# Kernel optimization log

Hardware: AMD Instinct MI355X
Metric: run time of the kernel (lower is better)

## Reference

```python
import jax, jax.numpy as jnp
import numpy as np

EMBED = 64
HEADS = 4
HEAD_DIM = EMBED // HEADS
N, T = 1024, 36


def setup_inputs() -> dict:
    key = jax.random.key(0)
    ks = jax.random.split(key, 8)
    scale = 1.0 / np.sqrt(HEAD_DIM)
    return {
        "values": jax.random.normal(ks[0], (N, T, EMBED), dtype=jnp.float32),
        "keys": jax.random.normal(ks[1], (N, T, EMBED), dtype=jnp.float32),
        "query": jax.random.normal(ks[2], (N, T, EMBED), dtype=jnp.float32),
        "Wv": jax.random.normal(ks[3], (HEAD_DIM, HEAD_DIM), dtype=jnp.float32) * scale,
        "Wk": jax.random.normal(ks[4], (HEAD_DIM, HEAD_DIM), dtype=jnp.float32) * scale,
        "Wq": jax.random.normal(ks[5], (HEAD_DIM, HEAD_DIM), dtype=jnp.float32) * scale,
        "Wo": jax.random.normal(ks[6], (EMBED, EMBED), dtype=jnp.float32) * (1.0 / np.sqrt(EMBED)),
        "bo": jax.random.normal(ks[7], (EMBED,), dtype=jnp.float32) * 0.01,
    }


def reference(values, keys, query, Wv, Wk, Wq, Wo, bo):
    n, t, c = query.shape
    h, d = HEADS, HEAD_DIM
    v = values.reshape(n, t, h, d)
    k = keys.reshape(n, t, h, d)
    q = query.reshape(n, t, h, d)
    # nn.Linear(head_dim, head_dim, bias=False): x @ W.T
    v = jnp.einsum('nthd,ed->nthe', v, Wv)
    k = jnp.einsum('nthd,ed->nthe', k, Wk)
    q = jnp.einsum('nthd,ed->nthe', q, Wq)
    # attention over the node dim: energy [N_q, N_k, T, H]
    energy = jnp.einsum('qthd,kthd->qkth', q, k)
    attention = jax.nn.softmax(energy / jnp.sqrt(jnp.float32(c)), axis=1)
    out = jnp.einsum('qkth,kthd->qthd', attention, v).reshape(n, t, h * d)
    return out @ Wo.T + bo
```

## Files before the change

### kernel.cpp

```cpp
#include <hip/hip_runtime.h>
#include <math.h>

#define N_NODES 1024
#define T_STEPS 36
#define KTILE   128
#define KSTR2   24
#define VTSTR   136
#define WOS     72
#define OBS2    72
#define YSTR    67

typedef __bf16  bf16x8 __attribute__((ext_vector_type(8)));
typedef float   f32x4  __attribute__((ext_vector_type(4)));

#define MFMA_BF16 __builtin_amdgcn_mfma_f32_16x16x32_bf16
#define PERM_HI 0x07060302u
#define PERM_LO 0x05040100u

__device__ __forceinline__ unsigned short bf16_rne(float f) {
    unsigned int u = __float_as_uint(f);
    u += 0x7FFFu + ((u >> 16) & 1u);
    return (unsigned short)(u >> 16);
}
__device__ __forceinline__ float bf16_tof(unsigned short h) {
    return __uint_as_float(((unsigned int)h) << 16);
}
__device__ __forceinline__ unsigned int bf16_bias(float f) {
    unsigned int u = __float_as_uint(f);
    return u + 0x7FFFu + ((u >> 16) & 1u);
}
__device__ __forceinline__ unsigned int split_pack(float a) {
    unsigned short hi = bf16_rne(a);
    unsigned short lo = bf16_rne(a - bf16_tof(hi));
    return ((unsigned int)hi << 16) | lo;
}

__global__ __launch_bounds__(128) void proj5_kernel(
    const float* __restrict__ vin, const float* __restrict__ kin, const float* __restrict__ qin,
    const float* __restrict__ Wv, const float* __restrict__ Wk, const float* __restrict__ Wq,
    unsigned short* __restrict__ qhi, unsigned short* __restrict__ qlo,
    unsigned short* __restrict__ khi, unsigned short* __restrict__ klo,
    unsigned short* __restrict__ vthi, unsigned short* __restrict__ vtlo)
{
    __shared__ float sW[256];
    __shared__ unsigned int ys[128 * YSTR];

    const int tid = threadIdx.x;
    const int mat = blockIdx.y;
    const int nt  = blockIdx.x & 15;
    const int tt  = blockIdx.x >> 4;
    const int n0  = nt * 64, t0 = tt * 2;

    const float* in = (mat == 0) ? vin : (mat == 1) ? kin : qin;
    const float* W  = (mat == 0) ? Wv  : (mat == 1) ? Wk  : Wq;
    sW[tid] = W[tid]; sW[tid + 128] = W[tid + 128];
    __syncthreads();

    {
        const int nl = tid >> 1, tl = tid & 1;
        const size_t p = ((size_t)(n0 + nl)) * T_STEPS + (t0 + tl);
        const float4* src = (const float4*)(in + p * 64);
        float x[64];
        #pragma unroll
        for (int i = 0; i < 16; ++i) {
            float4 f = src[i];
            x[4*i] = f.x; x[4*i+1] = f.y; x[4*i+2] = f.z; x[4*i+3] = f.w;
        }
        const float scale = (mat == 2) ? 0.18033688011112042f : 1.0f;
        unsigned int* yrow = &ys[tid * YSTR];
        #pragma unroll
        for (int e = 0; e < 16; ++e) {
            float4 w0 = *(const float4*)&sW[e*16+0],  w1 = *(const float4*)&sW[e*16+4];
            float4 w2 = *(const float4*)&sW[e*16+8],  w3 = *(const float4*)&sW[e*16+12];
            #pragma unroll
            for (int hd = 0; hd < 4; ++hd) {
                const float* xr = &x[hd*16];
                float a = xr[0]*w0.x;
                a = fmaf(xr[1],w0.y,a);  a = fmaf(xr[2],w0.z,a);  a = fmaf(xr[3],w0.w,a);
                a = fmaf(xr[4],w1.x,a);  a = fmaf(xr[5],w1.y,a);  a = fmaf(xr[6],w1.z,a);  a = fmaf(xr[7],w1.w,a);
                a = fmaf(xr[8],w2.x,a);  a = fmaf(xr[9],w2.y,a);  a = fmaf(xr[10],w2.z,a); a = fmaf(xr[11],w2.w,a);
                a = fmaf(xr[12],w3.x,a); a = fmaf(xr[13],w3.y,a); a = fmaf(xr[14],w3.z,a); a = fmaf(xr[15],w3.w,a);
                yrow[hd*16 + e] = split_pack(a * scale);
            }
        }
    }
    __syncthreads();

    if (mat != 0) {
        unsigned short* ohi = (mat == 1) ? khi : qhi;
        unsigned short* olo = (mat == 1) ? klo : qlo;
        const int nl2 = tid >> 1, eh = tid & 1;
        #pragma unroll
        for (int pass = 0; pass < 8; ++pass) {
            const int tl2 = pass & 1, hd = pass >> 1;
            const unsigned int* yr = &ys[(nl2*2 + tl2) * YSTR + hd*16 + eh*8];
            unsigned int u0 = yr[0], u1 = yr[1], u2 = yr[2], u3 = yr[3];
            unsigned int u4 = yr[4], u5 = yr[5], u6 = yr[6], u7 = yr[7];
            uint4 hi4, lo4;
            hi4.x = __builtin_amdgcn_perm(u1, u0, PERM_HI);
            hi4.y = __builtin_amdgcn_perm(u3, u2, PERM_HI);
            hi4.z = __builtin_amdgcn_perm(u5, u4, PERM_HI);
            hi4.w = __builtin_amdgcn_perm(u7, u6, PERM_HI);
            lo4.x = __builtin_amdgcn_perm(u1, u0, PERM_LO);
            lo4.y = __builtin_amdgcn_perm(u3, u2, PERM_LO);
            lo4.z = __builtin_amdgcn_perm(u5, u4, PERM_LO);
            lo4.w = __builtin_amdgcn_perm(u7, u6, PERM_LO);
            const int th = (t0 + tl2) * 4 + hd;
            const size_t off = ((size_t)th * N_NODES + n0 + nl2) * 16 + eh * 8;
            *(uint4*)(ohi + off) = hi4;
            *(uint4*)(olo + off) = lo4;
        }
    } else {
        const int e = tid >> 3, ng = tid & 7;
        #pragma unroll
        for (int pass = 0; pass < 8; ++pass) {
            const int tl2 = pass & 1, hd = pass >> 1;
            unsigned int u[8];
            #pragma unroll
            for (int j = 0; j < 8; ++j)
                u[j] = ys[((ng*8 + j)*2 + tl2) * YSTR + hd*16 + e];
            uint4 hi4, lo4;
            hi4.x = __builtin_amdgcn_perm(u[1], u[0], PERM_HI);
            hi4.y = __builtin_amdgcn_perm(u[3], u[2], PERM_HI);
            hi4.z = __builtin_amdgcn_perm(u[5], u[4], PERM_HI);
            hi4.w = __builtin_amdgcn_perm(u[7], u[6], PERM_HI);
            lo4.x = __builtin_amdgcn_perm(u[1], u[0], PERM_LO);
            lo4.y = __builtin_amdgcn_perm(u[3], u[2], PERM_LO);
            lo4.z = __builtin_amdgcn_perm(u[5], u[4], PERM_LO);
            lo4.w = __builtin_amdgcn_perm(u[7], u[6], PERM_LO);
            const int th = (t0 + tl2) * 4 + hd;
            const size_t off = ((size_t)th * 16 + e) * N_NODES + n0 + ng * 8;
            *(uint4*)(vthi + off) = hi4;
            *(uint4*)(vtlo + off) = lo4;
        }
    }
}

__global__ __launch_bounds__(256, 4) void attn_mfma3_kernel(
    const unsigned short* __restrict__ qhi, const unsigned short* __restrict__ qlo,
    const unsigned short* __restrict__ khi, const unsigned short* __restrict__ klo,
    const unsigned short* __restrict__ vthi, const unsigned short* __restrict__ vtlo,
    unsigned short* __restrict__ obh, unsigned short* __restrict__ obl)
{
    __shared__ unsigned short khi_s[KTILE * KSTR2];
    __shared__ unsigned short klo_s[KTILE * KSTR2];
    __shared__ unsigned short vthi_s[16 * VTSTR];
    __shared__ unsigned short vtlo_s[16 * VTSTR];

    const int tid  = threadIdx.x;
    const int wave = tid >> 6, lane = tid & 63;
    const int m = lane & 15, quad = lane >> 4;

    const int bid = blockIdx.x;
    const int th  = bid % 144;
    const int qb  = bid / 144;
    const int t   = th >> 2, hd = th & 3;
    const int q0  = qb * 128;
    const size_t base_th = (size_t)th * N_NODES;

    const bf16x8 bzero = {};
    bf16x8 b1q[2], b2q[2];
    #pragma unroll
    for (int g = 0; g < 2; ++g) {
        const int qrow = q0 + wave * 32 + g * 16 + m;
        b1q[g] = *(const bf16x8*)(qhi + (base_th + qrow) * 16 + (quad & 1) * 8);
        b2q[g] = (quad < 2)
            ? *(const bf16x8*)(qlo + (base_th + qrow) * 16 + (quad & 1) * 8) : bzero;
    }

    f32x4 og[2] = {{0.f,0.f,0.f,0.f},{0.f,0.f,0.f,0.f}};
    float lsum[2] = {0.f, 0.f};
    const unsigned short* kbase = (quad < 2) ? khi_s : klo_s;
    const int koff = m * KSTR2 + (quad & 1) * 8;
    const int voff = m * VTSTR + quad * 8;

    for (int kt = 0; kt < N_NODES; kt += KTILE) {
        __syncthreads();
        if (tid < 128) {
            const int r = tid;
            const uint4* gh = (const uint4*)(khi + (base_th + kt + r) * 16);
            const uint4* gl = (const uint4*)(klo + (base_th + kt + r) * 16);
            uint4 a0 = gh[0], a1 = gh[1], c0 = gl[0], c1 = gl[1];
            *(uint4*)&khi_s[r * KSTR2]     = a0;
            *(uint4*)&khi_s[r * KSTR2 + 8] = a1;
            *(uint4*)&klo_s[r * KSTR2]     = c0;
            *(uint4*)&klo_s[r * KSTR2 + 8] = c1;
        } else {
            const int j = tid - 128;
            const int sel = j >> 6, d = (j >> 2) & 15, part = j & 3;
            const unsigned short* src = (sel ? vtlo : vthi)
                + ((size_t)th * 16 + d) * N_NODES + kt + part * 32;
            unsigned short* dst = (sel ? vtlo_s : vthi_s) + d * VTSTR + part * 32;
            uint4 a0 = ((const uint4*)src)[0], a1 = ((const uint4*)src)[1];
            uint4 a2 = ((const uint4*)src)[2], a3 = ((const uint4*)src)[3];
            *(uint2*)&dst[0]  = make_uint2(a0.x, a0.y);
            *(uint2*)&dst[8]  = make_uint2(a0.z, a0.w);
            *(uint2*)&dst[16] = make_uint2(a1.x, a1.y);
            *(uint2*)&dst[24] = make_uint2(a1.z, a1.w);
            *(uint2*)&dst[4]  = make_uint2(a2.x, a2.y);
            *(uint2*)&dst[12] = make_uint2(a2.z, a2.w);
            *(uint2*)&dst[20] = make_uint2(a3.x, a3.y);
            *(uint2*)&dst[28] = make_uint2(a3.z, a3.w);
        }
        __syncthreads();

        #pragma unroll
        for (int c = 0; c < 4; ++c) {
            bf16x8 a0 = *(const bf16x8*)(kbase + (2*c    ) * 16 * KSTR2 + koff);
            bf16x8 a1 = *(const bf16x8*)(kbase + (2*c + 1) * 16 * KSTR2 + koff);
            unsigned int pk[2][4];
            #pragma unroll
            for (int g = 0; g < 2; ++g) {
                f32x4 s0 = MFMA_BF16(a0, b1q[g], (f32x4){0.f,0.f,0.f,0.f}, 0, 0, 0);
                s0 = MFMA_BF16(a0, b2q[g], s0, 0, 0, 0);
                f32x4 s1 = MFMA_BF16(a1, b1q[g], (f32x4){0.f,0.f,0.f,0.f}, 0, 0, 0);
                s1 = MFMA_BF16(a1, b2q[g], s1, 0, 0, 0);
                unsigned int u[8];
                float ls = 0.f;
                #pragma unroll
                for (int r = 0; r < 4; ++r) {
                    u[r]   = bf16_bias(__builtin_amdgcn_exp2f(s0[r]));
                    u[4+r] = bf16_bias(__builtin_amdgcn_exp2f(s1[r]));
                    ls += __uint_as_float(u[r]   & 0xFFFF0000u);
                    ls += __uint_as_float(u[4+r] & 0xFFFF0000u);
                }
                lsum[g] += ls;
                pk[g][0] = __builtin_amdgcn_perm(u[1], u[0], PERM_HI);
                pk[g][1] = __builtin_amdgcn_perm(u[3], u[2], PERM_HI);
                pk[g][2] = __builtin_amdgcn_perm(u[5], u[4], PERM_HI);
                pk[g][3] = __builtin_amdgcn_perm(u[7], u[6], PERM_HI);
            }
            bf16x8 vh = *(const bf16x8*)&vthi_s[voff + c * 32];
            bf16x8 vl = *(const bf16x8*)&vtlo_s[voff + c * 32];
            #pragma unroll
            for (int g = 0; g < 2; ++g) {
                union { unsigned int u[4]; bf16x8 v; } ap;
                ap.u[0] = pk[g][0]; ap.u[1] = pk[g][1];
                ap.u[2] = pk[g][2]; ap.u[3] = pk[g][3];
                og[g] = MFMA_BF16(ap.v, vh, og[g], 0, 0, 0);
                og[g] = MFMA_BF16(ap.v, vl, og[g], 0, 0, 0);
            }
        }
    }

    #pragma unroll
    for (int g = 0; g < 2; ++g) {
        lsum[g] += __shfl_xor(lsum[g], 16);
        lsum[g] += __shfl_xor(lsum[g], 32);
        #pragma unroll
        for (int r = 0; r < 4; ++r) {
            const float l = __shfl(lsum[g], quad * 4 + r);
            const float val = og[g][r] / l;
            const int row = q0 + wave * 32 + g * 16 + quad * 4 + r;
            const size_t off = ((size_t)row * T_STEPS + t) * 64 + hd * 16 + m;
            unsigned short hh = bf16_rne(val);
            obh[off] = hh;
            obl[off] = bf16_rne(val - bf16_tof(hh));
        }
    }
}

__global__ __launch_bounds__(256) void outproj_mfma_kernel(
    const unsigned short* __restrict__ obh, const unsigned short* __restrict__ obl,
    const float* __restrict__ Wo, const float* __restrict__ bo,
    float* __restrict__ out)
{
    __shared__ unsigned short woh[64 * WOS], wol[64 * WOS];
    __shared__ unsigned short oth[64 * OBS2], otl[64 * OBS2];
    __shared__ float sb[64];
    const int tid = threadIdx.x;

    #pragma unroll
    for (int i = 0; i < 16; ++i) {
        int idx = tid + 256 * i;
        int r = idx >> 6, c = idx & 63;
        float w = Wo[idx];
        unsigned short hh = bf16_rne(w);
        woh[r * WOS + c] = hh;
        wol[r * WOS + c] = bf16_rne(w - bf16_tof(hh));
    }
    if (tid < 64) sb[tid] = bo[tid];

    const size_t p0 = (size_t)blockIdx.x * 64;
    #pragma unroll
    for (int i = 0; i < 2; ++i) {
        int idx = tid + 256 * i;
        int r = idx >> 3, c = (idx & 7) * 8;
        *(uint4*)&oth[r * OBS2 + c] = *(const uint4*)(obh + (p0 + r) * 64 + c);
        *(uint4*)&otl[r * OBS2 + c] = *(const uint4*)(obl + (p0 + r) * 64 + c);
    }
    __syncthreads();

    const int wave = tid >> 6, lane = tid & 63;
    const int m = lane & 15, quad = lane >> 4;
    const int r0 = wave * 16;

    bf16x8 ah[2], al[2];
    #pragma unroll
    for (int kh = 0; kh < 2; ++kh) {
        ah[kh] = *(const bf16x8*)&oth[(r0 + m) * OBS2 + kh * 32 + quad * 8];
        al[kh] = *(const bf16x8*)&otl[(r0 + m) * OBS2 + kh * 32 + quad * 8];
    }

    f32x4 acc[4] = {{0,0,0,0},{0,0,0,0},{0,0,0,0},{0,0,0,0}};
    #pragma unroll
    for (int jt = 0; jt < 4; ++jt) {
        #pragma unroll
        for (int kh = 0; kh < 2; ++kh) {
            bf16x8 bh = *(const bf16x8*)&woh[(jt * 16 + m) * WOS + kh * 32 + quad * 8];
            bf16x8 bl = *(const bf16x8*)&wol[(jt * 16 + m) * WOS + kh * 32 + quad * 8];
            acc[jt] = MFMA_BF16(ah[kh], bh, acc[jt], 0, 0, 0);
            acc[jt] = MFMA_BF16(al[kh], bh, acc[jt], 0, 0, 0);
            acc[jt] = MFMA_BF16(ah[kh], bl, acc[jt], 0, 0, 0);
        }
    }

    #pragma unroll
    for (int jt = 0; jt < 4; ++jt) {
        const float b = sb[jt * 16 + m];
        #pragma unroll
        for (int r = 0; r < 4; ++r)
            out[(p0 + r0 + quad * 4 + r) * 64 + jt * 16 + m] = acc[jt][r] + b;
    }
}

extern "C" void kernel_launch(void* const* d_in, const int* in_sizes, int n_in,
                              void* d_out, int out_size, void* d_ws, size_t ws_size,
                              hipStream_t stream)
{
    (void)in_sizes; (void)n_in; (void)out_size; (void)ws_size;
    const float* values = (const float*)d_in[0];
    const float* keys   = (const float*)d_in[1];
    const float* query  = (const float*)d_in[2];
    const float* Wv     = (const float*)d_in[3];
    const float* Wk     = (const float*)d_in[4];
    const float* Wq     = (const float*)d_in[5];
    const float* Wo     = (const float*)d_in[6];
    const float* bo     = (const float*)d_in[7];

    const size_t TOT = (size_t)144 * N_NODES * 16;
    unsigned short* ws16 = (unsigned short*)d_ws;
    unsigned short* qhi  = ws16;
    unsigned short* qlo  = ws16 + 1*TOT;
    unsigned short* khi  = ws16 + 2*TOT;
    unsigned short* klo  = ws16 + 3*TOT;
    unsigned short* vthi = ws16 + 4*TOT;
    unsigned short* vtlo = ws16 + 5*TOT;
    unsigned short* obh  = ws16 + 6*TOT;
    unsigned short* obl  = ws16 + 7*TOT;

    proj5_kernel<<<dim3(288, 3), 128, 0, stream>>>(values, keys, query, Wv, Wk, Wq,
                                                   qhi, qlo, khi, klo, vthi, vtlo);
    attn_mfma3_kernel<<<dim3(8 * 144), 256, 0, stream>>>(qhi, qlo, khi, klo, vthi, vtlo,
                                                         obh, obl);
    outproj_mfma_kernel<<<dim3(576), 256, 0, stream>>>(obh, obl, Wo, bo, (float*)d_out);
}
```

Baseline: 145.9 us.

## Compute softmax row sums with MFMA against ones and halve attention block size

Row sums of the exponentials are now accumulated by an extra MFMA against a vector of bf16 ones, replacing the scalar adds and the cross-lane shuffles. The bias-add rounding and perm packing are replaced by direct __bf16 conversions. Blocks shrink to 128 threads and 64 queries each, with twice as many blocks, and both threads load K and V tiles. The trade-off is fewer queries sharing each K/V tile, which doubles K/V shared-memory staging traffic, plus one extra MFMA per group. The final division becomes a fast reciprocal multiply.

```diff
diff --git a/kernel.cpp b/kernel.cpp
--- a/kernel.cpp
+++ b/kernel.cpp
@@ -24,10 +24,6 @@
 }
 __device__ __forceinline__ float bf16_tof(unsigned short h) {
     return __uint_as_float(((unsigned int)h) << 16);
-}
-__device__ __forceinline__ unsigned int bf16_bias(float f) {
-    unsigned int u = __float_as_uint(f);
-    return u + 0x7FFFu + ((u >> 16) & 1u);
 }
 __device__ __forceinline__ unsigned int split_pack(float a) {
     unsigned short hi = bf16_rne(a);
@@ -136,7 +132,7 @@
     }
 }
 
-__global__ __launch_bounds__(256, 4) void attn_mfma3_kernel(
+__global__ __launch_bounds__(128, 4) void attn_mfma4_kernel(
     const unsigned short* __restrict__ qhi, const unsigned short* __restrict__ qlo,
     const unsigned short* __restrict__ khi, const unsigned short* __restrict__ klo,
     const unsigned short* __restrict__ vthi, const unsigned short* __restrict__ vtlo,
@@ -155,7 +151,7 @@
     const int th  = bid % 144;
     const int qb  = bid / 144;
     const int t   = th >> 2, hd = th & 3;
-    const int q0  = qb * 128;
+    const int q0  = qb * 64;
     const size_t base_th = (size_t)th * N_NODES;
 
     const bf16x8 bzero = {};
@@ -168,39 +164,45 @@
             ? *(const bf16x8*)(qlo + (base_th + qrow) * 16 + (quad & 1) * 8) : bzero;
     }
 
-    f32x4 og[2] = {{0.f,0.f,0.f,0.f},{0.f,0.f,0.f,0.f}};
-    float lsum[2] = {0.f, 0.f};
+    union { unsigned short su[8]; bf16x8 v; } onesu;
+    #pragma unroll
+    for (int i = 0; i < 8; ++i) onesu.su[i] = 0x3F80;
+    const bf16x8 bones = onesu.v;
+
+    f32x4 og[2]   = {{0.f,0.f,0.f,0.f},{0.f,0.f,0.f,0.f}};
+    f32x4 lacc[2] = {{0.f,0.f,0.f,0.f},{0.f,0.f,0.f,0.f}};
     const unsigned short* kbase = (quad < 2) ? khi_s : klo_s;
     const int koff = m * KSTR2 + (quad & 1) * 8;
     const int voff = m * VTSTR + quad * 8;
 
+    const int vsel = tid >> 6, vd = (tid >> 2) & 15, vpart = tid & 3;
+    const unsigned short* vsrc0 = (vsel ? vtlo : vthi)
+        + ((size_t)th * 16 + vd) * N_NODES + vpart * 32;
+    unsigned short* vdst = (vsel ? vtlo_s : vthi_s) + vd * VTSTR + vpart * 32;
+
     for (int kt = 0; kt < N_NODES; kt += KTILE) {
         __syncthreads();
-        if (tid < 128) {
-            const int r = tid;
-            const uint4* gh = (const uint4*)(khi + (base_th + kt + r) * 16);
-            const uint4* gl = (const uint4*)(klo + (base_th + kt + r) * 16);
+        {
+            const uint4* gh = (const uint4*)(khi + (base_th + kt + tid) * 16);
+            const uint4* gl = (const uint4*)(klo + (base_th + kt + tid) * 16);
             uint4 a0 = gh[0], a1 = gh[1], c0 = gl[0], c1 = gl[1];
-            *(uint4*)&khi_s[r * KSTR2]     = a0;
-            *(uint4*)&khi_s[r * KSTR2 + 8] = a1;
-            *(uint4*)&klo_s[r * KSTR2]     = c0;
-            *(uint4*)&klo_s[r * KSTR2 + 8] = c1;
-        } else {
-            const int j = tid - 128;
-            const int sel = j >> 6, d = (j >> 2) & 15, part = j & 3;
-            const unsigned short* src = (sel ? vtlo : vthi)
-                + ((size_t)th * 16 + d) * N_NODES + kt + part * 32;
-            unsigned short* dst = (sel ? vtlo_s : vthi_s) + d * VTSTR + part * 32;
+            *(uint4*)&khi_s[tid * KSTR2]     = a0;
+            *(uint4*)&khi_s[tid * KSTR2 + 8] = a1;
+            *(uint4*)&klo_s[tid * KSTR2]     = c0;
+            *(uint4*)&klo_s[tid * KSTR2 + 8] = c1;
+        }
+        {
+            const unsigned short* src = vsrc0 + kt;
             uint4 a0 = ((const uint4*)src)[0], a1 = ((const uint4*)src)[1];
             uint4 a2 = ((const uint4*)src)[2], a3 = ((const uint4*)src)[3];
-            *(uint2*)&dst[0]  = make_uint2(a0.x, a0.y);
-            *(uint2*)&dst[8]  = make_uint2(a0.z, a0.w);
-            *(uint2*)&dst[16] = make_uint2(a1.x, a1.y);
-            *(uint2*)&dst[24] = make_uint2(a1.z, a1.w);
-            *(uint2*)&dst[4]  = make_uint2(a2.x, a2.y);
-            *(uint2*)&dst[12] = make_uint2(a2.z, a2.w);
-            *(uint2*)&dst[20] = make_uint2(a3.x, a3.y);
-            *(uint2*)&dst[28] = make_uint2(a3.z, a3.w);
+            *(uint2*)&vdst[0]  = make_uint2(a0.x, a0.y);
+            *(uint2*)&vdst[8]  = make_uint2(a0.z, a0.w);
+            *(uint2*)&vdst[16] = make_uint2(a1.x, a1.y);
+            *(uint2*)&vdst[24] = make_uint2(a1.z, a1.w);
+            *(uint2*)&vdst[4]  = make_uint2(a2.x, a2.y);
+            *(uint2*)&vdst[12] = make_uint2(a2.z, a2.w);
+            *(uint2*)&vdst[20] = make_uint2(a3.x, a3.y);
+            *(uint2*)&vdst[28] = make_uint2(a3.z, a3.w);
         }
         __syncthreads();
 
@@ -208,49 +210,35 @@
         for (int c = 0; c < 4; ++c) {
             bf16x8 a0 = *(const bf16x8*)(kbase + (2*c    ) * 16 * KSTR2 + koff);
             bf16x8 a1 = *(const bf16x8*)(kbase + (2*c + 1) * 16 * KSTR2 + koff);
-            unsigned int pk[2][4];
+            bf16x8 vh = *(const bf16x8*)&vthi_s[voff + c * 32];
+            bf16x8 vl = *(const bf16x8*)&vtlo_s[voff + c * 32];
             #pragma unroll
             for (int g = 0; g < 2; ++g) {
                 f32x4 s0 = MFMA_BF16(a0, b1q[g], (f32x4){0.f,0.f,0.f,0.f}, 0, 0, 0);
                 s0 = MFMA_BF16(a0, b2q[g], s0, 0, 0, 0);
                 f32x4 s1 = MFMA_BF16(a1, b1q[g], (f32x4){0.f,0.f,0.f,0.f}, 0, 0, 0);
                 s1 = MFMA_BF16(a1, b2q[g], s1, 0, 0, 0);
-                unsigned int u[8];
-                float ls = 0.f;
-                #pragma unroll
-                for (int r = 0; r < 4; ++r) {
-                    u[r]   = bf16_bias(__builtin_amdgcn_exp2f(s0[r]));
-                    u[4+r] = bf16_bias(__builtin_amdgcn_exp2f(s1[r]));
-                    ls += __uint_as_float(u[r]   & 0xFFFF0000u);
-                    ls += __uint_as_float(u[4+r] & 0xFFFF0000u);
-                }
-                lsum[g] += ls;
-                pk[g][0] = __builtin_amdgcn_perm(u[1], u[0], PERM_HI);
-                pk[g][1] = __builtin_amdgcn_perm(u[3], u[2], PERM_HI);
-                pk[g][2] = __builtin_amdgcn_perm(u[5], u[4], PERM_HI);
-                pk[g][3] = __builtin_amdgcn_perm(u[7], u[6], PERM_HI);
+                union { __bf16 b[8]; bf16x8 v; } ap;
+                ap.b[0] = (__bf16)__builtin_amdgcn_exp2f(s0[0]);
+                ap.b[1] = (__bf16)__builtin_amdgcn_exp2f(s0[1]);
+                ap.b[2] = (__bf16)__builtin_amdgcn_exp2f(s0[2]);
+                ap.b[3] = (__bf16)__builtin_amdgcn_exp2f(s0[3]);
+                ap.b[4] = (__bf16)__builtin_amdgcn_exp2f(s1[0]);
+                ap.b[5] = (__bf16)__builtin_amdgcn_exp2f(s1[1]);
+                ap.b[6] = (__bf16)__builtin_amdgcn_exp2f(s1[2]);
+                ap.b[7] = (__bf16)__builtin_amdgcn_exp2f(s1[3]);
+                lacc[g] = MFMA_BF16(ap.v, bones, lacc[g], 0, 0, 0);
+                og[g]   = MFMA_BF16(ap.v, vh, og[g], 0, 0, 0);
+                og[g]   = MFMA_BF16(ap.v, vl, og[g], 0, 0, 0);
             }
-            bf16x8 vh = *(const bf16x8*)&vthi_s[voff + c * 32];
-            bf16x8 vl = *(const bf16x8*)&vtlo_s[voff + c * 32];
-            #pragma unroll
-            for (int g = 0; g < 2; ++g) {
-                union { unsigned int u[4]; bf16x8 v; } ap;
-                ap.u[0] = pk[g][0]; ap.u[1] = pk[g][1];
-                ap.u[2] = pk[g][2]; ap.u[3] = pk[g][3];
-                og[g] = MFMA_BF16(ap.v, vh, og[g], 0, 0, 0);
-                og[g] = MFMA_BF16(ap.v, vl, og[g], 0, 0, 0);
-            }
         }
     }
 
     #pragma unroll
     for (int g = 0; g < 2; ++g) {
-        lsum[g] += __shfl_xor(lsum[g], 16);
-        lsum[g] += __shfl_xor(lsum[g], 32);
         #pragma unroll
         for (int r = 0; r < 4; ++r) {
-            const float l = __shfl(lsum[g], quad * 4 + r);
-            const float val = og[g][r] / l;
+            const float val = og[g][r] * __builtin_amdgcn_rcpf(lacc[g][r]);
             const int row = q0 + wave * 32 + g * 16 + quad * 4 + r;
             const size_t off = ((size_t)row * T_STEPS + t) * 64 + hd * 16 + m;
             unsigned short hh = bf16_rne(val);
@@ -351,7 +339,7 @@
 
     proj5_kernel<<<dim3(288, 3), 128, 0, stream>>>(values, keys, query, Wv, Wk, Wq,
                                                    qhi, qlo, khi, klo, vthi, vtlo);
-    attn_mfma3_kernel<<<dim3(8 * 144), 256, 0, stream>>>(qhi, qlo, khi, klo, vthi, vtlo,
-                                                         obh, obl);
+    attn_mfma4_kernel<<<dim3(16 * 144), 128, 0, stream>>>(qhi, qlo, khi, klo, vthi, vtlo,
+                                                          obh, obl);
     outproj_mfma_kernel<<<dim3(576), 256, 0, stream>>>(obh, obl, Wo, bo, (float*)d_out);
 }
```

Result: faster. 138.0 us (-5.4%).
